# Performance work log

Measured on AMD Instinct MI355X. Metric: run time of the kernel, lower is better.

Reference implementation:

```python
import jax, jax.numpy as jnp
import numpy as np

H = 128          # hidden_size
B = 64           # batch of users
T = 20           # current-session length (== max_sess_len)
S = 10           # friend sessions per user (graph degree)
L = 20           # max_sess_len
NUM_ITEMS = 50000
NUM_USERS = 10000
TOPK = 2         # topk in sess_similarity


def gru(x, W_ih, W_hh, b_ih, b_hh):
    """torch nn.GRU (1 layer, batch_first). x: [N, T, H] -> outputs [N, T, H], h_T [N, H]."""
    h0 = jnp.zeros((x.shape[0], x.shape[-1]), x.dtype)

    def step(h, xt):
        gi = xt @ W_ih.T + b_ih          # [N, 3H]
        gh = h @ W_hh.T + b_hh
        i_r, i_z, i_n = jnp.split(gi, 3, axis=-1)
        h_r, h_z, h_n = jnp.split(gh, 3, axis=-1)
        r = jax.nn.sigmoid(i_r + h_r)
        z = jax.nn.sigmoid(i_z + h_z)
        n = jnp.tanh(i_n + r * h_n)
        h = (1.0 - z) * n + z * h
        return h, h

    hT, ys = jax.lax.scan(step, h0, jnp.swapaxes(x, 0, 1))
    return jnp.swapaxes(ys, 0, 1), hT


def masked_softmax(x, mask, axis):
    neg = jnp.finfo(x.dtype).min
    return jax.nn.softmax(jnp.where(mask, x, neg), axis=axis)


def setup_inputs() -> dict:
    key = jax.random.key(0)
    ks = jax.random.split(key, 12)
    users = jax.random.randint(ks[0], (B,), 0, NUM_USERS)
    cur_sess = jax.random.randint(ks[1], (B, T), 0, NUM_ITEMS)          # all valid -> full length
    hist_sess = jax.random.randint(ks[2], (B, S, L), 0, NUM_ITEMS)
    frds_sess = jax.random.randint(ks[3], (B, S, L), 0, NUM_ITEMS)
    cur_sess_len = jnp.full((B,), T, dtype=jnp.int32)
    # parameters
    v_emb = jax.random.uniform(ks[4], (NUM_ITEMS + 1, H), minval=-1.0, maxval=1.0)
    v_emb = v_emb.at[NUM_ITEMS].set(0.0)                                 # padding_idx row
    u_emb = jax.random.normal(ks[5], (NUM_USERS, H)) * (1.0 / np.sqrt(H))
    sc = 1.0 / np.sqrt(H)
    W_ih = jax.random.normal(ks[6], (3 * H, H)) * sc
    W_hh = jax.random.normal(ks[7], (3 * H, H)) * sc
    b_ih = jnp.zeros((3 * H,), jnp.float32)
    b_hh = jnp.zeros((3 * H,), jnp.float32)
    out1_w = jax.random.normal(ks[8], (NUM_ITEMS, 3 * H)) * (1.0 / np.sqrt(3 * H))
    out1_b = jnp.zeros((NUM_ITEMS,), jnp.float32)
    return dict(users=users, cur_sess=cur_sess, hist_sess=hist_sess, frds_sess=frds_sess,
                cur_sess_len=cur_sess_len, v_emb=v_emb, u_emb=u_emb,
                W_ih=W_ih, W_hh=W_hh, b_ih=b_ih, b_hh=b_hh, out1_w=out1_w, out1_b=out1_b)


def reference(users, cur_sess, hist_sess, frds_sess, cur_sess_len,
              v_emb, u_emb, W_ih, W_hh, b_ih, b_hh, out1_w, out1_b):
    # --- rnn_encoder on current session (dropout p=0, eval) ---
    hs, _ = gru(v_emb[cur_sess], W_ih, W_hh, b_ih, b_hh)                 # [B, T, H]
    query = hs

    # --- friend branch (hist branch is dead: hu is overwritten with zeros) ---
    # sess_encoder: GRU over each friend session's items
    frd_items = v_emb[frds_sess]                                         # [B, S, L, H]
    enc, _ = gru(frd_items.reshape(B * S, L, H), W_ih, W_hh, b_ih, b_hh)
    enc = enc.reshape(B, S, L, H)                                        # encoder_output

    # sess_similarity: max over session positions, softmax over degree (S)
    scores = jnp.einsum('bth,bslh->bstl', query, enc)                    # [B, S, T, L]
    sim_raw = scores.max(axis=-1)                                        # [B, S, T]
    sim1 = jax.nn.softmax(sim_raw, axis=1)
    # preserve: edges that are top-2 most similar for ANY step t (S > TOPK branch)
    _, idx = jax.lax.top_k(jnp.swapaxes(sim1, 1, 2), TOPK)               # [B, T, 2]
    preserve = jax.nn.one_hot(idx, S, dtype=jnp.float32).sum((1, 2)) > 0 # [B, S]

    # sess_embedding_attn on the filtered subgraph (masking == filtering here)
    user_e = u_emb[users]                                                # [B, H]
    w = jax.nn.softmax(jnp.einsum('bh,bslh->bsl', user_e, frd_items), axis=2)
    sess_emb = jnp.einsum('bsl,bslh->bsh', w, frd_items)                 # [B, S, H]

    # user_sess_reduce_func: sim1 (pre-filter softmax values), then two softmaxes
    # over the surviving edges (masked softmax over S)
    m = preserve[:, :, None]                                             # [B, S, 1]
    s = masked_softmax(sim1, m, axis=1)
    s = masked_softmax(s, m, axis=1)
    s = jnp.where(m, s, 0.0)
    hf = jnp.einsum('bst,bsh->bth', s, sess_emb)                         # [B, T, H]

    hu = jnp.zeros_like(hs)                                              # hu = zeros_like(hs)
    output = jnp.concatenate([hs, hu, hf], axis=-1)                      # [B, T, 3H]
    logits = output @ out1_w.T + out1_b                                  # [B, T, NUM_ITEMS]
    return logits
```

## Files before the change

### kernel.cpp

```cpp
#include <hip/hip_runtime.h>
#include <cstdint>
#include <cstddef>

#define H_      128
#define B_      64
#define T_      20
#define S_      10
#define L_      20
#define NITEMS  50000
#define NSEQ    704
#define NTOK    (NSEQ * 20)
#define NPAD    50048
#define KA      256

typedef __attribute__((ext_vector_type(8))) short short8;
typedef __attribute__((ext_vector_type(4))) float f32x4;

__device__ __forceinline__ unsigned short f2bf(float f) {
  unsigned int u = __float_as_uint(f);
  u += 0x7FFF + ((u >> 16) & 1);
  return (unsigned short)(u >> 16);
}
__device__ __forceinline__ float sigmoidf_(float x) {
  return 1.0f / (1.0f + __expf(-x));
}

__global__ void __launch_bounds__(256) k1_convert_w(const float* __restrict__ w,
                                                    unsigned short* __restrict__ wb) {
  int t = blockIdx.x * 256 + threadIdx.x;
  int n = t >> 5, kc = t & 31;
  int k0 = kc * 8;
  unsigned int o0, o1, o2, o3;
  if (n < NITEMS) {
    int src = (k0 < 128) ? k0 : (k0 + 128);
    const float* p = w + (size_t)n * 384 + src;
    float4 f0 = *(const float4*)p;
    float4 f1 = *(const float4*)(p + 4);
    o0 = (unsigned)f2bf(f0.x) | ((unsigned)f2bf(f0.y) << 16);
    o1 = (unsigned)f2bf(f0.z) | ((unsigned)f2bf(f0.w) << 16);
    o2 = (unsigned)f2bf(f1.x) | ((unsigned)f2bf(f1.y) << 16);
    o3 = (unsigned)f2bf(f1.z) | ((unsigned)f2bf(f1.w) << 16);
  } else {
    o0 = o1 = o2 = o3 = 0u;
  }
  *(uint4*)(wb + (size_t)n * 256 + k0) = make_uint4(o0, o1, o2, o3);
}

__global__ void __launch_bounds__(384) k2_gi(const int* __restrict__ cur,
                                             const int* __restrict__ frd,
                                             const float* __restrict__ vemb,
                                             const float* __restrict__ Wih,
                                             const float* __restrict__ bih,
                                             float* __restrict__ gi) {
  __shared__ float xs[16 * 128];
  __shared__ int ids[16];
  int tid = threadIdx.x;
  int tok0 = blockIdx.x * 16;
  if (tid < 16) {
    int tok = tok0 + tid;
    int seq = tok / 20, tt = tok % 20;
    ids[tid] = (seq < 64) ? cur[seq * 20 + tt] : frd[(seq - 64) * 20 + tt];
  }
  __syncthreads();
  for (int idx = tid; idx < 512; idx += 384) {
    int i = idx >> 5, kc = idx & 31;
    *(float4*)&xs[i * 128 + kc * 4] =
        *(const float4*)&vemb[(size_t)ids[i] * 128 + kc * 4];
  }
  __syncthreads();
  int j = tid;
  float acc[16];
#pragma unroll
  for (int i = 0; i < 16; i++) acc[i] = 0.f;
  const float* wrow = Wih + (size_t)j * 128;
  for (int kc = 0; kc < 32; kc++) {
    float4 w4 = *(const float4*)(wrow + kc * 4);
#pragma unroll
    for (int i = 0; i < 16; i++) {
      float4 x4 = *(const float4*)&xs[i * 128 + kc * 4];
      acc[i] += w4.x * x4.x + w4.y * x4.y + w4.z * x4.z + w4.w * x4.w;
    }
  }
  float bb = bih[j];
#pragma unroll
  for (int i = 0; i < 16; i++)
    gi[(size_t)(tok0 + i) * 384 + j] = acc[i] + bb;
}

__global__ void __launch_bounds__(384) k3_gru(const float* __restrict__ Whh,
                                              const float* __restrict__ bhh,
                                              const float* __restrict__ gi,
                                              float* __restrict__ out_h) {
  __shared__ float hb[3 * 128];
  __shared__ float pre[3 * 256];
  __shared__ float gin[3 * 128];
  __shared__ float ghn[3 * 128];
  int j = threadIdx.x;
  int seq0 = blockIdx.x * 3;
  int G = NSEQ - seq0; if (G > 3) G = 3;
  float4 wv[32];
  const float4* wr = (const float4*)(Whh + (size_t)j * 128);
#pragma unroll
  for (int kc = 0; kc < 32; kc++) wv[kc] = wr[kc];
  float bb = bhh[j];
  if (j < 128) { hb[j] = 0.f; hb[128 + j] = 0.f; hb[256 + j] = 0.f; }
  __syncthreads();
  for (int t = 0; t < 20; t++) {
    for (int g = 0; g < G; g++) {
      float acc = bb;
#pragma unroll
      for (int kc = 0; kc < 32; kc++) {
        float4 h4 = *(const float4*)&hb[g * 128 + kc * 4];
        float4 w4 = wv[kc];
        acc += w4.x * h4.x + w4.y * h4.y + w4.z * h4.z + w4.w * h4.w;
      }
      float gv = gi[(size_t)((seq0 + g) * 20 + t) * 384 + j];
      if (j < 256) pre[g * 256 + j] = gv + acc;
      else { gin[g * 128 + (j - 256)] = gv; ghn[g * 128 + (j - 256)] = acc; }
    }
    __syncthreads();
    if (j < 128) {
      for (int g = 0; g < G; g++) {
        float r = sigmoidf_(pre[g * 256 + j]);
        float z = sigmoidf_(pre[g * 256 + 128 + j]);
        float n = tanhf(gin[g * 128 + j] + r * ghn[g * 128 + j]);
        float hN = (1.f - z) * n + z * hb[g * 128 + j];
        hb[g * 128 + j] = hN;
        out_h[(size_t)((seq0 + g) * 20 + t) * 128 + j] = hN;
      }
    }
    __syncthreads();
  }
}

__global__ void __launch_bounds__(256) k4_scores(const float* __restrict__ out_h,
                                                 float* __restrict__ sim_raw) {
  __shared__ float qs[20 * 132];
  __shared__ float es[20 * 132];
  __shared__ float sc[400];
  int tid = threadIdx.x;
  int b = blockIdx.x / 10, s = blockIdx.x % 10;
  int eseq = 64 + b * 10 + s;
  for (int idx = tid; idx < 640; idx += 256) {
    int row = idx >> 5, kc = idx & 31;
    *(float4*)&qs[row * 132 + kc * 4] =
        *(const float4*)&out_h[(size_t)(b * 20 + row) * 128 + kc * 4];
    *(float4*)&es[row * 132 + kc * 4] =
        *(const float4*)&out_h[(size_t)(eseq * 20 + row) * 128 + kc * 4];
  }
  __syncthreads();
  for (int idx = tid; idx < 400; idx += 256) {
    int t = idx / 20, l = idx % 20;
    float acc = 0.f;
#pragma unroll
    for (int kc = 0; kc < 32; kc++) {
      float4 q4 = *(const float4*)&qs[t * 132 + kc * 4];
      float4 e4 = *(const float4*)&es[l * 132 + kc * 4];
      acc += q4.x * e4.x + q4.y * e4.y + q4.z * e4.z + q4.w * e4.w;
    }
    sc[idx] = acc;
  }
  __syncthreads();
  if (tid < 20) {
    float m = sc[tid * 20];
    for (int l = 1; l < 20; l++) m = fmaxf(m, sc[tid * 20 + l]);
    sim_raw[(size_t)(b * 10 + s) * 20 + tid] = m;
  }
}

__global__ void __launch_bounds__(64) k5_soft(const float* __restrict__ sim_raw,
                                              float* __restrict__ sfin) {
  __shared__ float sv[200];
  __shared__ float s1[200];
  __shared__ int pres[10];
  int tid = threadIdx.x;
  int b = blockIdx.x;
  for (int idx = tid; idx < 200; idx += 64) sv[idx] = sim_raw[(size_t)b * 200 + idx];
  if (tid < 10) pres[tid] = 0;
  __syncthreads();
  if (tid < 20) {
    int t = tid;
    float mx = -3.4e38f;
    for (int s = 0; s < 10; s++) mx = fmaxf(mx, sv[s * 20 + t]);
    float sum = 0.f;
    for (int s = 0; s < 10; s++) sum += __expf(sv[s * 20 + t] - mx);
    float inv = 1.0f / sum;
    float v1 = -1.f, v2 = -1.f; int i1 = 0, i2 = 0;
    for (int s = 0; s < 10; s++) {
      float v = __expf(sv[s * 20 + t] - mx) * inv;
      s1[s * 20 + t] = v;
      if (v > v1) { v2 = v1; i2 = i1; v1 = v; i1 = s; }
      else if (v > v2) { v2 = v; i2 = s; }
    }
    atomicOr(&pres[i1], 1);
    atomicOr(&pres[i2], 1);
  }
  __syncthreads();
  if (tid < 20) {
    int t = tid;
    float mx = -3.4e38f;
    for (int s = 0; s < 10; s++) if (pres[s]) mx = fmaxf(mx, s1[s * 20 + t]);
    float sum = 0.f;
    for (int s = 0; s < 10; s++) if (pres[s]) sum += __expf(s1[s * 20 + t] - mx);
    float inv = 1.f / sum;
    float mx2 = -3.4e38f;
    for (int s = 0; s < 10; s++)
      if (pres[s]) mx2 = fmaxf(mx2, __expf(s1[s * 20 + t] - mx) * inv);
    float sum2 = 0.f;
    for (int s = 0; s < 10; s++)
      if (pres[s]) sum2 += __expf(__expf(s1[s * 20 + t] - mx) * inv - mx2);
    float inv2 = 1.f / sum2;
    for (int s = 0; s < 10; s++) {
      float o = 0.f;
      if (pres[s]) o = __expf(__expf(s1[s * 20 + t] - mx) * inv - mx2) * inv2;
      sfin[(size_t)(b * 10 + s) * 20 + t] = o;
    }
  }
}

__global__ void __launch_bounds__(128) k6_sess(const int* __restrict__ users,
                                               const int* __restrict__ frd,
                                               const float* __restrict__ vemb,
                                               const float* __restrict__ uemb,
                                               float* __restrict__ sess) {
  __shared__ float fs[20 * 132];
  __shared__ float us[128];
  __shared__ float dt[20];
  __shared__ float wl[20];
  __shared__ int fid[20];
  int tid = threadIdx.x;
  int b = blockIdx.x / 10, s = blockIdx.x % 10;
  if (tid < 20) fid[tid] = frd[(size_t)(b * 10 + s) * 20 + tid];
  us[tid] = uemb[(size_t)users[b] * 128 + tid];
  __syncthreads();
  for (int idx = tid; idx < 640; idx += 128) {
    int row = idx >> 5, kc = idx & 31;
    *(float4*)&fs[row * 132 + kc * 4] =
        *(const float4*)&vemb[(size_t)fid[row] * 128 + kc * 4];
  }
  __syncthreads();
  if (tid < 20) {
    float acc = 0.f;
    for (int kc = 0; kc < 32; kc++) {
      float4 u4 = *(const float4*)&us[kc * 4];
      float4 f4 = *(const float4*)&fs[tid * 132 + kc * 4];
      acc += u4.x * f4.x + u4.y * f4.y + u4.z * f4.z + u4.w * f4.w;
    }
    dt[tid] = acc;
  }
  __syncthreads();
  if (tid < 20) {
    float mx = -3.4e38f;
    for (int l = 0; l < 20; l++) mx = fmaxf(mx, dt[l]);
    float sum = 0.f;
    for (int l = 0; l < 20; l++) sum += __expf(dt[l] - mx);
    wl[tid] = __expf(dt[tid] - mx) / sum;
  }
  __syncthreads();
  float acc = 0.f;
  for (int l = 0; l < 20; l++) acc += wl[l] * fs[l * 132 + tid];
  sess[(size_t)(b * 10 + s) * 128 + tid] = acc;
}

__global__ void __launch_bounds__(256) k7_hf(const float* __restrict__ sfin,
                                             const float* __restrict__ sess,
                                             float* __restrict__ hf) {
  __shared__ float sf[200];
  __shared__ float se[10 * 128];
  int tid = threadIdx.x;
  int b = blockIdx.x;
  for (int idx = tid; idx < 200; idx += 256) sf[idx] = sfin[(size_t)b * 200 + idx];
  for (int idx = tid; idx < 1280; idx += 256) se[idx] = sess[(size_t)b * 1280 + idx];
  __syncthreads();
  for (int idx = tid; idx < 2560; idx += 256) {
    int t = idx >> 7, h = idx & 127;
    float acc = 0.f;
#pragma unroll
    for (int s = 0; s < 10; s++) acc += sf[s * 20 + t] * se[s * 128 + h];
    hf[(size_t)b * 2560 + idx] = acc;
  }
}

__global__ void __launch_bounds__(256) k8_act(const float* __restrict__ out_h,
                                              const float* __restrict__ hf,
                                              unsigned int* __restrict__ act) {
  int g = blockIdx.x * 256 + threadIdx.x;
  int m = g >> 7, p = g & 127;
  float a0, a1;
  if (p < 64) {
    a0 = out_h[(size_t)m * 128 + p * 2];
    a1 = out_h[(size_t)m * 128 + p * 2 + 1];
  } else {
    a0 = hf[(size_t)m * 128 + (p - 64) * 2];
    a1 = hf[(size_t)m * 128 + (p - 64) * 2 + 1];
  }
  act[g] = (unsigned)f2bf(a0) | ((unsigned)f2bf(a1) << 16);
}

__device__ __forceinline__ void async_cp16(const unsigned short* g, unsigned short* l) {
  __builtin_amdgcn_global_load_lds((__attribute__((address_space(1))) void*)g,
                                   (__attribute__((address_space(3))) void*)l,
                                   16, 0, 0);
}

__global__ void __launch_bounds__(256) k9_gemm(const unsigned short* __restrict__ act,
                                               const unsigned short* __restrict__ wb,
                                               const float* __restrict__ bias,
                                               float* __restrict__ out) {
  __shared__ __align__(16) unsigned short Bs[128 * 256];
  __shared__ __align__(16) unsigned short As[128 * 40];
  int tid = threadIdx.x;
  int w = tid >> 6, lane = tid & 63;
  int q = (lane >> 4) & 3, c = lane & 15;
  int wm = w >> 1, wn = w & 1;
  int nb0 = blockIdx.x * 128;

#pragma unroll
  for (int i = 0; i < 16; i++) {
    int n_l = i * 8 + w * 2 + (lane >> 5);
    int p = lane & 31;
    int kc = p ^ (n_l & 31);
    async_cp16(wb + (size_t)(nb0 + n_l) * 256 + kc * 8,
               &Bs[(i * 8 + w * 2) * 256]);
  }

  float bs[4]; int okn[4]; int ncol[4];
#pragma unroll
  for (int nt = 0; nt < 4; nt++) {
    int n = nb0 + wn * 64 + nt * 16 + c;
    ncol[nt] = n;
    okn[nt] = (n < NITEMS);
    bs[nt] = (n < NITEMS) ? bias[n] : 0.f;
  }

  for (int mc = 0; mc < 10; mc++) {
    f32x4 acc[4][4];
#pragma unroll
    for (int mt = 0; mt < 4; mt++)
#pragma unroll
      for (int nt = 0; nt < 4; nt++) {
        f32x4 z = {0.f, 0.f, 0.f, 0.f};
        acc[mt][nt] = z;
      }
    for (int kf = 0; kf < 8; kf++) {
      __syncthreads();
      {
        int ch0 = tid * 2;
#pragma unroll
        for (int jj = 0; jj < 2; jj++) {
          int ch = ch0 + jj;
          int row = ch >> 2, kk = ch & 3;
          short8 v = *(const short8*)&act[(size_t)(mc * 128 + row) * 256 + kf * 32 + kk * 8];
          *(short8*)&As[row * 40 + kk * 8] = v;
        }
      }
      __syncthreads();
      short8 bfr[4];
#pragma unroll
      for (int nt = 0; nt < 4; nt++) {
        int n_l = wn * 64 + nt * 16 + c;
        int slot = n_l * 32 + ((kf * 4 + q) ^ (n_l & 31));
        bfr[nt] = *(const short8*)&Bs[slot * 8];
      }
#pragma unroll
      for (int mt = 0; mt < 4; mt++) {
        int row = wm * 64 + mt * 16 + c;
        short8 af = *(const short8*)&As[row * 40 + q * 8];
#pragma unroll
        for (int nt = 0; nt < 4; nt++)
          acc[mt][nt] = __builtin_amdgcn_mfma_f32_16x16x32_bf16(af, bfr[nt], acc[mt][nt], 0, 0, 0);
      }
    }
#pragma unroll
    for (int nt = 0; nt < 4; nt++) {
      if (okn[nt]) {
#pragma unroll
        for (int mt = 0; mt < 4; mt++) {
          int m = mc * 128 + wm * 64 + mt * 16 + q * 4;
#pragma unroll
          for (int r = 0; r < 4; r++)
            out[(size_t)(m + r) * NITEMS + ncol[nt]] = acc[mt][nt][r] + bs[nt];
        }
      }
    }
  }
}

extern "C" void kernel_launch(void* const* d_in, const int* in_sizes, int n_in,
                              void* d_out, int out_size, void* d_ws, size_t ws_size,
                              hipStream_t stream) {
  const int*   users = (const int*)d_in[0];
  const int*   cur   = (const int*)d_in[1];
  const int*   frd   = (const int*)d_in[3];
  const float* vemb  = (const float*)d_in[5];
  const float* uemb  = (const float*)d_in[6];
  const float* Wih   = (const float*)d_in[7];
  const float* Whh   = (const float*)d_in[8];
  const float* bih   = (const float*)d_in[9];
  const float* bhh   = (const float*)d_in[10];
  const float* w1    = (const float*)d_in[11];
  const float* b1    = (const float*)d_in[12];
  float* out = (float*)d_out;

  char* ws = (char*)d_ws;
  size_t off = 0;
  auto alloc = [&](size_t bytes) -> void* {
    void* p = ws + off;
    off = (off + bytes + 255) & ~(size_t)255;
    return p;
  };
  unsigned short* wb   = (unsigned short*)alloc((size_t)NPAD * 256 * 2);
  unsigned int*   act  = (unsigned int*)alloc((size_t)1280 * 128 * 4);
  float*          gi   = (float*)alloc((size_t)NTOK * 384 * 4);
  float*          outh = (float*)alloc((size_t)NTOK * 128 * 4);
  float*          simr = (float*)alloc((size_t)12800 * 4);
  float*          sfin = (float*)alloc((size_t)12800 * 4);
  float*          sess = (float*)alloc((size_t)640 * 128 * 4);
  float*          hf   = (float*)alloc((size_t)1280 * 128 * 4);

  k1_convert_w<<<NPAD / 8, 256, 0, stream>>>(w1, wb);
  k2_gi<<<NTOK / 16, 384, 0, stream>>>(cur, frd, vemb, Wih, bih, gi);
  k3_gru<<<(NSEQ + 2) / 3, 384, 0, stream>>>(Whh, bhh, gi, outh);
  k4_scores<<<640, 256, 0, stream>>>(outh, simr);
  k5_soft<<<64, 64, 0, stream>>>(simr, sfin);
  k6_sess<<<640, 128, 0, stream>>>(users, frd, vemb, uemb, sess);
  k7_hf<<<64, 256, 0, stream>>>(sfin, sess, hf);
  k8_act<<<640, 256, 0, stream>>>(outh, hf, act);
  k9_gemm<<<NPAD / 128, 256, 0, stream>>>((const unsigned short*)act, wb, b1, out);
}
```

Baseline: 523.2 us.

## Fuse attention stages and weight conversion into fewer kernels, one sequence per GRU block

Merges the score, softmax, session-embedding, hf and activation-packing kernels into a single per-user kernel, and folds the fp32-to-bf16 weight conversion into the GEMM's LDS fill. The GEMM now reads A fragments straight from global memory instead of staging them through LDS with barriers. The GRU kernel is changed to process one sequence per block instead of three. This removes several launches and intermediate global round-trips, including the separate bf16 weight buffer. In exchange the fused attention kernel runs only 64 blocks with serial loops over sessions, and the GRU launches more blocks that each reload the recurrent weights into registers.

```diff
diff --git a/kernel.cpp b/kernel.cpp
--- a/kernel.cpp
+++ b/kernel.cpp
@@ -3,15 +3,10 @@
 #include <cstddef>
 
 #define H_      128
-#define B_      64
-#define T_      20
-#define S_      10
-#define L_      20
 #define NITEMS  50000
 #define NSEQ    704
 #define NTOK    (NSEQ * 20)
 #define NPAD    50048
-#define KA      256
 
 typedef __attribute__((ext_vector_type(8))) short short8;
 typedef __attribute__((ext_vector_type(4))) float f32x4;
@@ -25,28 +20,7 @@
   return 1.0f / (1.0f + __expf(-x));
 }
 
-__global__ void __launch_bounds__(256) k1_convert_w(const float* __restrict__ w,
-                                                    unsigned short* __restrict__ wb) {
-  int t = blockIdx.x * 256 + threadIdx.x;
-  int n = t >> 5, kc = t & 31;
-  int k0 = kc * 8;
-  unsigned int o0, o1, o2, o3;
-  if (n < NITEMS) {
-    int src = (k0 < 128) ? k0 : (k0 + 128);
-    const float* p = w + (size_t)n * 384 + src;
-    float4 f0 = *(const float4*)p;
-    float4 f1 = *(const float4*)(p + 4);
-    o0 = (unsigned)f2bf(f0.x) | ((unsigned)f2bf(f0.y) << 16);
-    o1 = (unsigned)f2bf(f0.z) | ((unsigned)f2bf(f0.w) << 16);
-    o2 = (unsigned)f2bf(f1.x) | ((unsigned)f2bf(f1.y) << 16);
-    o3 = (unsigned)f2bf(f1.z) | ((unsigned)f2bf(f1.w) << 16);
-  } else {
-    o0 = o1 = o2 = o3 = 0u;
-  }
-  *(uint4*)(wb + (size_t)n * 256 + k0) = make_uint4(o0, o1, o2, o3);
-}
-
-__global__ void __launch_bounds__(384) k2_gi(const int* __restrict__ cur,
+__global__ void __launch_bounds__(384) kA_gi(const int* __restrict__ cur,
                                              const int* __restrict__ frd,
                                              const float* __restrict__ vemb,
                                              const float* __restrict__ Wih,
@@ -87,107 +61,148 @@
     gi[(size_t)(tok0 + i) * 384 + j] = acc[i] + bb;
 }
 
-__global__ void __launch_bounds__(384) k3_gru(const float* __restrict__ Whh,
+__global__ void __launch_bounds__(384) kB_gru(const float* __restrict__ Whh,
                                               const float* __restrict__ bhh,
                                               const float* __restrict__ gi,
                                               float* __restrict__ out_h) {
-  __shared__ float hb[3 * 128];
-  __shared__ float pre[3 * 256];
-  __shared__ float gin[3 * 128];
-  __shared__ float ghn[3 * 128];
+  __shared__ float hb[128];
+  __shared__ float pre[256];
+  __shared__ float gin[128];
+  __shared__ float ghn[128];
   int j = threadIdx.x;
-  int seq0 = blockIdx.x * 3;
-  int G = NSEQ - seq0; if (G > 3) G = 3;
+  int seq = blockIdx.x;
   float4 wv[32];
   const float4* wr = (const float4*)(Whh + (size_t)j * 128);
 #pragma unroll
   for (int kc = 0; kc < 32; kc++) wv[kc] = wr[kc];
   float bb = bhh[j];
-  if (j < 128) { hb[j] = 0.f; hb[128 + j] = 0.f; hb[256 + j] = 0.f; }
+  if (j < 128) hb[j] = 0.f;
   __syncthreads();
   for (int t = 0; t < 20; t++) {
-    for (int g = 0; g < G; g++) {
-      float acc = bb;
-#pragma unroll
-      for (int kc = 0; kc < 32; kc++) {
-        float4 h4 = *(const float4*)&hb[g * 128 + kc * 4];
-        float4 w4 = wv[kc];
-        acc += w4.x * h4.x + w4.y * h4.y + w4.z * h4.z + w4.w * h4.w;
-      }
-      float gv = gi[(size_t)((seq0 + g) * 20 + t) * 384 + j];
-      if (j < 256) pre[g * 256 + j] = gv + acc;
-      else { gin[g * 128 + (j - 256)] = gv; ghn[g * 128 + (j - 256)] = acc; }
-    }
+    float acc = bb;
+#pragma unroll
+    for (int kc = 0; kc < 32; kc++) {
+      float4 h4 = *(const float4*)&hb[kc * 4];
+      float4 w4 = wv[kc];
+      acc += w4.x * h4.x + w4.y * h4.y + w4.z * h4.z + w4.w * h4.w;
+    }
+    float gv = gi[(size_t)(seq * 20 + t) * 384 + j];
+    if (j < 256) pre[j] = gv + acc;
+    else { gin[j - 256] = gv; ghn[j - 256] = acc; }
     __syncthreads();
     if (j < 128) {
-      for (int g = 0; g < G; g++) {
-        float r = sigmoidf_(pre[g * 256 + j]);
-        float z = sigmoidf_(pre[g * 256 + 128 + j]);
-        float n = tanhf(gin[g * 128 + j] + r * ghn[g * 128 + j]);
-        float hN = (1.f - z) * n + z * hb[g * 128 + j];
-        hb[g * 128 + j] = hN;
-        out_h[(size_t)((seq0 + g) * 20 + t) * 128 + j] = hN;
-      }
-    }
-    __syncthreads();
-  }
-}
-
-__global__ void __launch_bounds__(256) k4_scores(const float* __restrict__ out_h,
-                                                 float* __restrict__ sim_raw) {
-  __shared__ float qs[20 * 132];
-  __shared__ float es[20 * 132];
+      float r = sigmoidf_(pre[j]);
+      float z = sigmoidf_(pre[128 + j]);
+      float n = tanhf(gin[j] + r * ghn[j]);
+      float hN = (1.f - z) * n + z * hb[j];
+      hb[j] = hN;
+      out_h[(size_t)(seq * 20 + t) * 128 + j] = hN;
+    }
+    __syncthreads();
+  }
+}
+
+__global__ void __launch_bounds__(256) kC_attn(const int* __restrict__ users,
+                                               const int* __restrict__ frd,
+                                               const float* __restrict__ vemb,
+                                               const float* __restrict__ uemb,
+                                               const float* __restrict__ outh,
+                                               unsigned int* __restrict__ act) {
+  __shared__ float hs[20 * 132];
+  __shared__ float buf[20 * 132];
   __shared__ float sc[400];
-  int tid = threadIdx.x;
-  int b = blockIdx.x / 10, s = blockIdx.x % 10;
-  int eseq = 64 + b * 10 + s;
-  for (int idx = tid; idx < 640; idx += 256) {
-    int row = idx >> 5, kc = idx & 31;
-    *(float4*)&qs[row * 132 + kc * 4] =
-        *(const float4*)&out_h[(size_t)(b * 20 + row) * 128 + kc * 4];
-    *(float4*)&es[row * 132 + kc * 4] =
-        *(const float4*)&out_h[(size_t)(eseq * 20 + row) * 128 + kc * 4];
-  }
-  __syncthreads();
-  for (int idx = tid; idx < 400; idx += 256) {
-    int t = idx / 20, l = idx % 20;
-    float acc = 0.f;
-#pragma unroll
-    for (int kc = 0; kc < 32; kc++) {
-      float4 q4 = *(const float4*)&qs[t * 132 + kc * 4];
-      float4 e4 = *(const float4*)&es[l * 132 + kc * 4];
-      acc += q4.x * e4.x + q4.y * e4.y + q4.z * e4.z + q4.w * e4.w;
-    }
-    sc[idx] = acc;
-  }
-  __syncthreads();
-  if (tid < 20) {
-    float m = sc[tid * 20];
-    for (int l = 1; l < 20; l++) m = fmaxf(m, sc[tid * 20 + l]);
-    sim_raw[(size_t)(b * 10 + s) * 20 + tid] = m;
-  }
-}
-
-__global__ void __launch_bounds__(64) k5_soft(const float* __restrict__ sim_raw,
-                                              float* __restrict__ sfin) {
-  __shared__ float sv[200];
+  __shared__ float sim[200];
   __shared__ float s1[200];
+  __shared__ float sfin[200];
+  __shared__ float sess[10 * 128];
+  __shared__ float us[128];
+  __shared__ float dt[20];
+  __shared__ float wl[20];
   __shared__ int pres[10];
   int tid = threadIdx.x;
   int b = blockIdx.x;
-  for (int idx = tid; idx < 200; idx += 64) sv[idx] = sim_raw[(size_t)b * 200 + idx];
+
+  for (int idx = tid; idx < 640; idx += 256) {
+    int row = idx >> 5, kc = idx & 31;
+    *(float4*)&hs[row * 132 + kc * 4] =
+        *(const float4*)&outh[(size_t)(b * 20 + row) * 128 + kc * 4];
+  }
+  if (tid < 128) us[tid] = uemb[(size_t)users[b] * 128 + tid];
   if (tid < 10) pres[tid] = 0;
   __syncthreads();
+
+  for (int s = 0; s < 10; s++) {
+    int eseq = 64 + b * 10 + s;
+    for (int idx = tid; idx < 640; idx += 256) {
+      int row = idx >> 5, kc = idx & 31;
+      *(float4*)&buf[row * 132 + kc * 4] =
+          *(const float4*)&outh[(size_t)(eseq * 20 + row) * 128 + kc * 4];
+    }
+    __syncthreads();
+    for (int idx = tid; idx < 400; idx += 256) {
+      int t = idx / 20, l = idx % 20;
+      float acc = 0.f;
+#pragma unroll
+      for (int kc = 0; kc < 32; kc++) {
+        float4 q4 = *(const float4*)&hs[t * 132 + kc * 4];
+        float4 e4 = *(const float4*)&buf[l * 132 + kc * 4];
+        acc += q4.x * e4.x + q4.y * e4.y + q4.z * e4.z + q4.w * e4.w;
+      }
+      sc[idx] = acc;
+    }
+    __syncthreads();
+    if (tid < 20) {
+      float m = sc[tid * 20];
+      for (int l = 1; l < 20; l++) m = fmaxf(m, sc[tid * 20 + l]);
+      sim[s * 20 + tid] = m;
+    }
+    __syncthreads();
+  }
+
+  for (int s = 0; s < 10; s++) {
+    for (int idx = tid; idx < 640; idx += 256) {
+      int row = idx >> 5, kc = idx & 31;
+      int fid = frd[(size_t)(b * 10 + s) * 20 + row];
+      *(float4*)&buf[row * 132 + kc * 4] =
+          *(const float4*)&vemb[(size_t)fid * 128 + kc * 4];
+    }
+    __syncthreads();
+    if (tid < 20) {
+      float acc = 0.f;
+      for (int kc = 0; kc < 32; kc++) {
+        float4 u4 = *(const float4*)&us[kc * 4];
+        float4 f4 = *(const float4*)&buf[tid * 132 + kc * 4];
+        acc += u4.x * f4.x + u4.y * f4.y + u4.z * f4.z + u4.w * f4.w;
+      }
+      dt[tid] = acc;
+    }
+    __syncthreads();
+    if (tid < 20) {
+      float mx = -3.4e38f;
+      for (int l = 0; l < 20; l++) mx = fmaxf(mx, dt[l]);
+      float sum = 0.f;
+      for (int l = 0; l < 20; l++) sum += __expf(dt[l] - mx);
+      wl[tid] = __expf(dt[tid] - mx) / sum;
+    }
+    __syncthreads();
+    if (tid < 128) {
+      float acc = 0.f;
+      for (int l = 0; l < 20; l++) acc += wl[l] * buf[l * 132 + tid];
+      sess[s * 128 + tid] = acc;
+    }
+    __syncthreads();
+  }
+
   if (tid < 20) {
     int t = tid;
     float mx = -3.4e38f;
-    for (int s = 0; s < 10; s++) mx = fmaxf(mx, sv[s * 20 + t]);
+    for (int s = 0; s < 10; s++) mx = fmaxf(mx, sim[s * 20 + t]);
     float sum = 0.f;
-    for (int s = 0; s < 10; s++) sum += __expf(sv[s * 20 + t] - mx);
+    for (int s = 0; s < 10; s++) sum += __expf(sim[s * 20 + t] - mx);
     float inv = 1.0f / sum;
     float v1 = -1.f, v2 = -1.f; int i1 = 0, i2 = 0;
     for (int s = 0; s < 10; s++) {
-      float v = __expf(sv[s * 20 + t] - mx) * inv;
+      float v = __expf(sim[s * 20 + t] - mx) * inv;
       s1[s * 20 + t] = v;
       if (v > v1) { v2 = v1; i2 = i1; v1 = v; i1 = s; }
       else if (v > v2) { v2 = v; i2 = s; }
@@ -213,102 +228,38 @@
     for (int s = 0; s < 10; s++) {
       float o = 0.f;
       if (pres[s]) o = __expf(__expf(s1[s * 20 + t] - mx) * inv - mx2) * inv2;
-      sfin[(size_t)(b * 10 + s) * 20 + t] = o;
-    }
-  }
-}
-
-__global__ void __launch_bounds__(128) k6_sess(const int* __restrict__ users,
-                                               const int* __restrict__ frd,
-                                               const float* __restrict__ vemb,
-                                               const float* __restrict__ uemb,
-                                               float* __restrict__ sess) {
-  __shared__ float fs[20 * 132];
-  __shared__ float us[128];
-  __shared__ float dt[20];
-  __shared__ float wl[20];
-  __shared__ int fid[20];
-  int tid = threadIdx.x;
-  int b = blockIdx.x / 10, s = blockIdx.x % 10;
-  if (tid < 20) fid[tid] = frd[(size_t)(b * 10 + s) * 20 + tid];
-  us[tid] = uemb[(size_t)users[b] * 128 + tid];
-  __syncthreads();
-  for (int idx = tid; idx < 640; idx += 128) {
-    int row = idx >> 5, kc = idx & 31;
-    *(float4*)&fs[row * 132 + kc * 4] =
-        *(const float4*)&vemb[(size_t)fid[row] * 128 + kc * 4];
-  }
-  __syncthreads();
-  if (tid < 20) {
-    float acc = 0.f;
-    for (int kc = 0; kc < 32; kc++) {
-      float4 u4 = *(const float4*)&us[kc * 4];
-      float4 f4 = *(const float4*)&fs[tid * 132 + kc * 4];
-      acc += u4.x * f4.x + u4.y * f4.y + u4.z * f4.z + u4.w * f4.w;
-    }
-    dt[tid] = acc;
-  }
-  __syncthreads();
-  if (tid < 20) {
-    float mx = -3.4e38f;
-    for (int l = 0; l < 20; l++) mx = fmaxf(mx, dt[l]);
-    float sum = 0.f;
-    for (int l = 0; l < 20; l++) sum += __expf(dt[l] - mx);
-    wl[tid] = __expf(dt[tid] - mx) / sum;
-  }
-  __syncthreads();
-  float acc = 0.f;
-  for (int l = 0; l < 20; l++) acc += wl[l] * fs[l * 132 + tid];
-  sess[(size_t)(b * 10 + s) * 128 + tid] = acc;
-}
-
-__global__ void __launch_bounds__(256) k7_hf(const float* __restrict__ sfin,
-                                             const float* __restrict__ sess,
-                                             float* __restrict__ hf) {
-  __shared__ float sf[200];
-  __shared__ float se[10 * 128];
-  int tid = threadIdx.x;
-  int b = blockIdx.x;
-  for (int idx = tid; idx < 200; idx += 256) sf[idx] = sfin[(size_t)b * 200 + idx];
-  for (int idx = tid; idx < 1280; idx += 256) se[idx] = sess[(size_t)b * 1280 + idx];
-  __syncthreads();
+      sfin[s * 20 + t] = o;
+    }
+  }
+  __syncthreads();
+
   for (int idx = tid; idx < 2560; idx += 256) {
-    int t = idx >> 7, h = idx & 127;
-    float acc = 0.f;
-#pragma unroll
-    for (int s = 0; s < 10; s++) acc += sf[s * 20 + t] * se[s * 128 + h];
-    hf[(size_t)b * 2560 + idx] = acc;
-  }
-}
-
-__global__ void __launch_bounds__(256) k8_act(const float* __restrict__ out_h,
-                                              const float* __restrict__ hf,
-                                              unsigned int* __restrict__ act) {
-  int g = blockIdx.x * 256 + threadIdx.x;
-  int m = g >> 7, p = g & 127;
-  float a0, a1;
-  if (p < 64) {
-    a0 = out_h[(size_t)m * 128 + p * 2];
-    a1 = out_h[(size_t)m * 128 + p * 2 + 1];
-  } else {
-    a0 = hf[(size_t)m * 128 + (p - 64) * 2];
-    a1 = hf[(size_t)m * 128 + (p - 64) * 2 + 1];
-  }
-  act[g] = (unsigned)f2bf(a0) | ((unsigned)f2bf(a1) << 16);
-}
-
-__device__ __forceinline__ void async_cp16(const unsigned short* g, unsigned short* l) {
-  __builtin_amdgcn_global_load_lds((__attribute__((address_space(1))) void*)g,
-                                   (__attribute__((address_space(3))) void*)l,
-                                   16, 0, 0);
-}
-
-__global__ void __launch_bounds__(256) k9_gemm(const unsigned short* __restrict__ act,
-                                               const unsigned short* __restrict__ wb,
+    int t = idx >> 7, u = idx & 127;
+    float a0, a1;
+    if (u < 64) {
+      a0 = hs[t * 132 + u * 2];
+      a1 = hs[t * 132 + u * 2 + 1];
+    } else {
+      int h0 = (u - 64) * 2;
+      float s0 = 0.f, s1v = 0.f;
+#pragma unroll
+      for (int s = 0; s < 10; s++) {
+        float w = sfin[s * 20 + t];
+        s0 += w * sess[s * 128 + h0];
+        s1v += w * sess[s * 128 + h0 + 1];
+      }
+      a0 = s0; a1 = s1v;
+    }
+    act[(size_t)(b * 20 + t) * 128 + u] =
+        (unsigned)f2bf(a0) | ((unsigned)f2bf(a1) << 16);
+  }
+}
+
+__global__ void __launch_bounds__(256) kD_gemm(const unsigned short* __restrict__ act,
+                                               const float* __restrict__ w1,
                                                const float* __restrict__ bias,
                                                float* __restrict__ out) {
   __shared__ __align__(16) unsigned short Bs[128 * 256];
-  __shared__ __align__(16) unsigned short As[128 * 40];
   int tid = threadIdx.x;
   int w = tid >> 6, lane = tid & 63;
   int q = (lane >> 4) & 3, c = lane & 15;
@@ -316,12 +267,20 @@
   int nb0 = blockIdx.x * 128;
 
 #pragma unroll
-  for (int i = 0; i < 16; i++) {
-    int n_l = i * 8 + w * 2 + (lane >> 5);
-    int p = lane & 31;
-    int kc = p ^ (n_l & 31);
-    async_cp16(wb + (size_t)(nb0 + n_l) * 256 + kc * 8,
-               &Bs[(i * 8 + w * 2) * 256]);
+  for (int it = 0; it < 32; it++) {
+    int idx = it * 256 + tid;
+    int n_l = idx >> 6, ch = idx & 63;
+    int n = nb0 + n_l;
+    int c4 = ch * 4;
+    int src = (c4 < 128) ? c4 : (c4 + 128);
+    float4 f;
+    if (n < NITEMS) f = *(const float4*)&w1[(size_t)n * 384 + src];
+    else { f.x = 0.f; f.y = 0.f; f.z = 0.f; f.w = 0.f; }
+    unsigned int lo = (unsigned)f2bf(f.x) | ((unsigned)f2bf(f.y) << 16);
+    unsigned int hi = (unsigned)f2bf(f.z) | ((unsigned)f2bf(f.w) << 16);
+    int kc16 = ch >> 1, half = ch & 1;
+    int p = kc16 ^ (n_l & 31);
+    *(uint2*)&Bs[n_l * 256 + p * 8 + half * 4] = make_uint2(lo, hi);
   }
 
   float bs[4]; int okn[4]; int ncol[4];
@@ -332,6 +291,7 @@
     okn[nt] = (n < NITEMS);
     bs[nt] = (n < NITEMS) ? bias[n] : 0.f;
   }
+  __syncthreads();
 
   for (int mc = 0; mc < 10; mc++) {
     f32x4 acc[4][4];
@@ -342,19 +302,14 @@
         f32x4 z = {0.f, 0.f, 0.f, 0.f};
         acc[mt][nt] = z;
       }
+#pragma unroll
     for (int kf = 0; kf < 8; kf++) {
-      __syncthreads();
-      {
-        int ch0 = tid * 2;
-#pragma unroll
-        for (int jj = 0; jj < 2; jj++) {
-          int ch = ch0 + jj;
-          int row = ch >> 2, kk = ch & 3;
-          short8 v = *(const short8*)&act[(size_t)(mc * 128 + row) * 256 + kf * 32 + kk * 8];
-          *(short8*)&As[row * 40 + kk * 8] = v;
-        }
-      }
-      __syncthreads();
+      short8 afr[4];
+#pragma unroll
+      for (int mt = 0; mt < 4; mt++) {
+        int row = mc * 128 + wm * 64 + mt * 16 + c;
+        afr[mt] = *(const short8*)&act[(size_t)row * 256 + kf * 32 + q * 8];
+      }
       short8 bfr[4];
 #pragma unroll
       for (int nt = 0; nt < 4; nt++) {
@@ -363,13 +318,10 @@
         bfr[nt] = *(const short8*)&Bs[slot * 8];
       }
 #pragma unroll
-      for (int mt = 0; mt < 4; mt++) {
-        int row = wm * 64 + mt * 16 + c;
-        short8 af = *(const short8*)&As[row * 40 + q * 8];
+      for (int mt = 0; mt < 4; mt++)
 #pragma unroll
         for (int nt = 0; nt < 4; nt++)
-          acc[mt][nt] = __builtin_amdgcn_mfma_f32_16x16x32_bf16(af, bfr[nt], acc[mt][nt], 0, 0, 0);
-      }
+          acc[mt][nt] = __builtin_amdgcn_mfma_f32_16x16x32_bf16(afr[mt], bfr[nt], acc[mt][nt], 0, 0, 0);
     }
 #pragma unroll
     for (int nt = 0; nt < 4; nt++) {
@@ -409,22 +361,12 @@
     off = (off + bytes + 255) & ~(size_t)255;
     return p;
   };
-  unsigned short* wb   = (unsigned short*)alloc((size_t)NPAD * 256 * 2);
-  unsigned int*   act  = (unsigned int*)alloc((size_t)1280 * 128 * 4);
-  float*          gi   = (float*)alloc((size_t)NTOK * 384 * 4);
-  float*          outh = (float*)alloc((size_t)NTOK * 128 * 4);
-  float*          simr = (float*)alloc((size_t)12800 * 4);
-  float*          sfin = (float*)alloc((size_t)12800 * 4);
-  float*          sess = (float*)alloc((size_t)640 * 128 * 4);
-  float*          hf   = (float*)alloc((size_t)1280 * 128 * 4);
-
-  k1_convert_w<<<NPAD / 8, 256, 0, stream>>>(w1, wb);
-  k2_gi<<<NTOK / 16, 384, 0, stream>>>(cur, frd, vemb, Wih, bih, gi);
-  k3_gru<<<(NSEQ + 2) / 3, 384, 0, stream>>>(Whh, bhh, gi, outh);
-  k4_scores<<<640, 256, 0, stream>>>(outh, simr);
-  k5_soft<<<64, 64, 0, stream>>>(simr, sfin);
-  k6_sess<<<640, 128, 0, stream>>>(users, frd, vemb, uemb, sess);
-  k7_hf<<<64, 256, 0, stream>>>(sfin, sess, hf);
-  k8_act<<<640, 256, 0, stream>>>(outh, hf, act);
-  k9_gemm<<<NPAD / 128, 256, 0, stream>>>((const unsigned short*)act, wb, b1, out);
-}
+  float*        gi   = (float*)alloc((size_t)NTOK * 384 * 4);
+  float*        outh = (float*)alloc((size_t)NTOK * 128 * 4);
+  unsigned int* act  = (unsigned int*)alloc((size_t)1280 * 128 * 4);
+
+  kA_gi<<<NTOK / 16, 384, 0, stream>>>(cur, frd, vemb, Wih, bih, gi);
+  kB_gru<<<NSEQ, 384, 0, stream>>>(Whh, bhh, gi, outh);
+  kC_attn<<<64, 256, 0, stream>>>(users, frd, vemb, uemb, outh, act);
+  kD_gemm<<<NPAD / 128, 256, 0, stream>>>((const unsigned short*)act, w1, b1, out);
+}
```

Measured after the change: 634.9 us. 21.3% more time.
